# Kernel optimization log

Measured on AMD Instinct MI355X. Metric: run time of the kernel, lower is better.

Reference implementation:

```python
import math
import jax, jax.numpy as jnp
import numpy as np

H = 16  # num_attention_heads
EPS = 1e-6

def _rmsnorm(x, w):
    xf = x.astype(jnp.float32)
    y = xf * jax.lax.rsqrt(jnp.mean(xf * xf, axis=-1, keepdims=True) + EPS)
    return (y * w).astype(x.dtype)

def setup_inputs() -> dict:
    key = jax.random.key(0)
    ks = jax.random.split(key, 4)
    B, S, D = 4, 1536, 2048
    return {
        "x": jax.random.normal(ks[0], (B, S, D), jnp.float32),
        "w_qkv": jax.random.normal(ks[1], (D, 3 * D), jnp.float32) * (1.0 / math.sqrt(D)),
        "b_qkv": jnp.zeros((3 * D,), jnp.float32),
        "q_ln_w": jnp.ones((D,), jnp.float32),
        "k_ln_w": jnp.ones((D,), jnp.float32),
        "w_out": jax.random.normal(ks[2], (D, D), jnp.float32) * (1.0 / math.sqrt(D)),
        "b_out": jnp.zeros((D,), jnp.float32),
    }

def reference(x, w_qkv, b_qkv, q_ln_w, k_ln_w, w_out, b_out):
    B, S, D = x.shape
    hd = D // H
    scale = 1.0 / math.sqrt(hd)
    qkv = x @ w_qkv + b_qkv                     # [B,S,3D]
    q, k, v = jnp.split(qkv, 3, axis=-1)
    q = _rmsnorm(q, q_ln_w)                     # QK-RMSNorm over hidden dim
    k = _rmsnorm(k, k_ln_w)
    # [B,S,D] -> [B,H,S,hd]
    q = q.reshape(B, S, H, hd).transpose(0, 2, 1, 3)
    k = k.reshape(B, S, H, hd).transpose(0, 2, 1, 3)
    v = v.reshape(B, S, H, hd).transpose(0, 2, 1, 3)
    scores = jnp.einsum('bhqd,bhkd->bhqk', q, k) * scale
    min_val = jnp.finfo(scores.dtype).min
    causal = jnp.tril(jnp.ones((S, S), dtype=bool))
    scores = jnp.where(causal[None, None], scores, min_val)
    probs = jax.nn.softmax(scores, axis=-1)
    out = jnp.einsum('bhqk,bhkd->bhqd', probs, v)
    out = out.transpose(0, 2, 1, 3).reshape(B, S, D)
    return out @ w_out + b_out
```

## Files before the change

### kernel.cpp

```cpp
#include <hip/hip_runtime.h>
#include <stdint.h>

#define BB 4
#define SS 1536
#define DD 2048
#define HH 16
#define HD 128
#define BS (BB * SS)
#define N3 (3 * DD)

typedef __bf16 bf16x8 __attribute__((ext_vector_type(8)));
typedef float f32x4 __attribute__((ext_vector_type(4)));

__device__ __forceinline__ void async16(const void* g, void* lds) {
  __builtin_amdgcn_global_load_lds(
      (const __attribute__((address_space(1))) unsigned int*)g,
      (__attribute__((address_space(3))) unsigned int*)lds, 16, 0, 0);
}

__global__ __launch_bounds__(256) void cast_bf16_kernel(
    const float* __restrict__ in, __bf16* __restrict__ out) {
  long i = ((long)blockIdx.x * 256 + threadIdx.x) * 8;
  float4 a = *(const float4*)(in + i);
  float4 b = *(const float4*)(in + i + 4);
  bf16x8 o;
  o[0] = (__bf16)a.x; o[1] = (__bf16)a.y; o[2] = (__bf16)a.z; o[3] = (__bf16)a.w;
  o[4] = (__bf16)b.x; o[5] = (__bf16)b.y; o[6] = (__bf16)b.z; o[7] = (__bf16)b.w;
  *(bf16x8*)(out + i) = o;
}

__global__ __launch_bounds__(256) void transpose_cast_kernel(
    const float* __restrict__ in, __bf16* __restrict__ out, int R, int C) {
  __shared__ __bf16 t[32][33];
  int tx = threadIdx.x & 31, ty = threadIdx.x >> 5;
  long r0 = (long)blockIdx.y * 32, c0 = (long)blockIdx.x * 32;
#pragma unroll
  for (int i = 0; i < 4; ++i)
    t[ty + i * 8][tx] = (__bf16)in[(r0 + ty + i * 8) * C + c0 + tx];
  __syncthreads();
#pragma unroll
  for (int i = 0; i < 4; ++i)
    out[(c0 + ty + i * 8) * R + r0 + tx] = t[tx][ty + i * 8];
}

__device__ __forceinline__ void store_val(__bf16* p, float v) { *p = (__bf16)v; }
__device__ __forceinline__ void store_val(float* p, float v) { *p = v; }

#define MFMA_PRE()                                          \
  __builtin_amdgcn_s_barrier();                             \
  asm volatile("s_waitcnt lgkmcnt(0)" ::: "memory");        \
  __builtin_amdgcn_sched_barrier(0);                        \
  __builtin_amdgcn_s_setprio(1)
#define MFMA_POST()                                         \
  __builtin_amdgcn_s_setprio(0);                            \
  __builtin_amdgcn_s_barrier()
#define MFMA16(AF, BF, IOFF, JOFF)                                          \
  _Pragma("unroll") for (int i_ = 0; i_ < 4; ++i_)                          \
  _Pragma("unroll") for (int j_ = 0; j_ < 2; ++j_)                          \
  _Pragma("unroll") for (int kk_ = 0; kk_ < 2; ++kk_)                       \
    acc[(IOFF) + i_][(JOFF) + j_] = __builtin_amdgcn_mfma_f32_16x16x32_bf16( \
        AF[i_][kk_], BF[j_][kk_], acc[(IOFF) + i_][(JOFF) + j_], 0, 0, 0)

template <typename OutT>
__global__ __launch_bounds__(512, 2) void gemm256_kernel(
    const __bf16* __restrict__ A, const __bf16* __restrict__ Bt,
    const float* __restrict__ bias, OutT* __restrict__ C,
    int M, int N, int K) {
  __shared__ __attribute__((aligned(16))) __bf16 sA[2][2][128 * 64];
  __shared__ __attribute__((aligned(16))) __bf16 sB[2][2][128 * 64];

  const int tid = threadIdx.x;
  const int wave = tid >> 6, lane = tid & 63;
  const int quad = lane >> 4, l15 = lane & 15;
  const int s7 = l15 & 7;
  const int wm = wave >> 2, wn = wave & 3;

  const int nwg = gridDim.x;
  int wg = (int)blockIdx.x;
  wg = (wg & 7) * (nwg >> 3) + (wg >> 3);
  const int NB = N >> 8;
  const int bm = (wg / NB) << 8;
  const int bn = (wg % NB) << 8;

  const int srow = lane >> 3;
  const int schunk = (lane & 7) ^ srow;
  const __bf16* aSrc[2][2];
  const __bf16* bSrc[2][2];
#pragma unroll
  for (int h = 0; h < 2; ++h)
#pragma unroll
    for (int t8 = 0; t8 < 2; ++t8) {
      int rl = wave * 16 + t8 * 8 + srow;
      aSrc[h][t8] = A + (long)(bm + h * 128 + rl) * K + schunk * 8;
      bSrc[h][t8] = Bt + (long)(bn + h * 128 + rl) * K + schunk * 8;
    }

  auto stageA = [&](int kt, int b, int h) {
#pragma unroll
    for (int t8 = 0; t8 < 2; ++t8)
      async16(aSrc[h][t8] + kt * 64, &sA[b][h][(wave * 16 + t8 * 8) * 64]);
  };
  auto stageB = [&](int kt, int b, int h) {
#pragma unroll
    for (int t8 = 0; t8 < 2; ++t8)
      async16(bSrc[h][t8] + kt * 64, &sB[b][h][(wave * 16 + t8 * 8) * 64]);
  };
  auto readA = [&](int b, int i, int kk) -> bf16x8 {
    return *(const bf16x8*)&sA[b][wm]
        [(i * 16 + l15) * 64 + (((kk * 4 + quad) ^ s7) * 8)];
  };
  auto readB = [&](int b, int j, int kk) -> bf16x8 {
    return *(const bf16x8*)&sB[b][wn >> 1]
        [((wn & 1) * 64 + j * 16 + l15) * 64 + (((kk * 4 + quad) ^ s7) * 8)];
  };

  f32x4 acc[8][4] = {};

  stageA(0, 0, 0); stageA(0, 0, 1); stageB(0, 0, 0); stageB(0, 0, 1);
  stageA(1, 1, 0); stageA(1, 1, 1); stageB(1, 1, 0);
  asm volatile("s_waitcnt vmcnt(6)" ::: "memory");
  __builtin_amdgcn_s_barrier();

  const int NT = K >> 6;
  bf16x8 af[4][2], af2[4][2], bf[2][2], bf2[2][2];

#pragma unroll 1
  for (int t = 0; t < NT; t += 2) {
    const bool full = (t + 2) < NT;

#pragma unroll
    for (int i = 0; i < 4; ++i) { af[i][0] = readA(0, i, 0); af[i][1] = readA(0, i, 1); }
#pragma unroll
    for (int j = 0; j < 2; ++j) { bf[j][0] = readB(0, j, 0); bf[j][1] = readB(0, j, 1); }
    stageB(t + 1, 1, 1);
    MFMA_PRE();
    MFMA16(af, bf, 0, 0);
    MFMA_POST();

#pragma unroll
    for (int i = 0; i < 4; ++i) { af2[i][0] = readA(0, 4 + i, 0); af2[i][1] = readA(0, 4 + i, 1); }
    MFMA_PRE();
    MFMA16(af2, bf, 4, 0);
    MFMA_POST();

#pragma unroll
    for (int j = 0; j < 2; ++j) { bf2[j][0] = readB(0, 2 + j, 0); bf2[j][1] = readB(0, 2 + j, 1); }
    if (full) stageA(t + 2, 0, 0);
    MFMA_PRE();
    MFMA16(af2, bf2, 4, 2);
    MFMA_POST();

    if (full) {
      stageA(t + 2, 0, 1);
      stageB(t + 2, 0, 0);
      asm volatile("s_waitcnt vmcnt(6)" ::: "memory");
    } else {
      asm volatile("s_waitcnt vmcnt(0)" ::: "memory");
    }
    MFMA_PRE();
    MFMA16(af, bf2, 0, 2);
    MFMA_POST();

#pragma unroll
    for (int i = 0; i < 4; ++i) { af[i][0] = readA(1, i, 0); af[i][1] = readA(1, i, 1); }
#pragma unroll
    for (int j = 0; j < 2; ++j) { bf[j][0] = readB(1, j, 0); bf[j][1] = readB(1, j, 1); }
    if (full) stageB(t + 2, 0, 1);
    MFMA_PRE();
    MFMA16(af, bf, 0, 0);
    MFMA_POST();

#pragma unroll
    for (int i = 0; i < 4; ++i) { af2[i][0] = readA(1, 4 + i, 0); af2[i][1] = readA(1, 4 + i, 1); }
    MFMA_PRE();
    MFMA16(af2, bf, 4, 0);
    MFMA_POST();

#pragma unroll
    for (int j = 0; j < 2; ++j) { bf2[j][0] = readB(1, 2 + j, 0); bf2[j][1] = readB(1, 2 + j, 1); }
    if (full) stageA(t + 3, 1, 0);
    MFMA_PRE();
    MFMA16(af2, bf2, 4, 2);
    MFMA_POST();

    if (full) {
      stageA(t + 3, 1, 1);
      stageB(t + 3, 1, 0);
      asm volatile("s_waitcnt vmcnt(6)" ::: "memory");
    } else {
      asm volatile("s_waitcnt vmcnt(0)" ::: "memory");
    }
    MFMA_PRE();
    MFMA16(af, bf2, 0, 2);
    MFMA_POST();
  }

#pragma unroll
  for (int i = 0; i < 8; ++i) {
    int row0 = bm + wm * 128 + i * 16 + quad * 4;
#pragma unroll
    for (int j = 0; j < 4; ++j) {
      int col = bn + wn * 64 + j * 16 + l15;
      float bv = bias[col];
#pragma unroll
      for (int r = 0; r < 4; ++r)
        store_val(&C[(long)(row0 + r) * N + col], acc[i][j][r] + bv);
    }
  }
}

__global__ __launch_bounds__(256) void rmsnorm_kernel(
    __bf16* __restrict__ qkv, const float* __restrict__ qw,
    const float* __restrict__ kw) {
  const int r = blockIdx.x;
  const bool isQ = r < BS;
  const int row = isQ ? r : r - BS;
  __bf16* p = qkv + (long)row * N3 + (isQ ? 0 : DD);
  const float* w = isQ ? qw : kw;
  const float extra = isQ ? (0.0883883476483184f * 1.44269504088896f) : 1.0f;
  const int t = threadIdx.x;

  bf16x8 v = *(const bf16x8*)(p + t * 8);
  float f[8];
  float s = 0.f;
#pragma unroll
  for (int i = 0; i < 8; ++i) { f[i] = (float)v[i]; s += f[i] * f[i]; }
#pragma unroll
  for (int off = 32; off > 0; off >>= 1) s += __shfl_xor(s, off, 64);
  __shared__ float red[4];
  if ((t & 63) == 0) red[t >> 6] = s;
  __syncthreads();
  float tot = red[0] + red[1] + red[2] + red[3];
  float rs = rsqrtf(tot * (1.0f / (float)DD) + 1e-6f) * extra;
  bf16x8 o;
#pragma unroll
  for (int i = 0; i < 8; ++i) o[i] = (__bf16)(f[i] * rs * w[t * 8 + i]);
  *(bf16x8*)(p + t * 8) = o;
}

__global__ __launch_bounds__(256) void transpose_v_kernel(
    const __bf16* __restrict__ qkv, __bf16* __restrict__ vt) {
  __shared__ __bf16 t[32][33];
  const int bh = blockIdx.z, b = bh >> 4, h = bh & 15;
  const int s0 = blockIdx.x * 32, d0 = blockIdx.y * 32;
  const int tx = threadIdx.x & 31, ty = threadIdx.x >> 5;
#pragma unroll
  for (int i = 0; i < 4; ++i) {
    int s = s0 + ty + i * 8;
    t[ty + i * 8][tx] =
        qkv[(long)(b * SS + s) * N3 + 2 * DD + h * HD + d0 + tx];
  }
  __syncthreads();
#pragma unroll
  for (int i = 0; i < 4; ++i) {
    int d = d0 + ty + i * 8;
    vt[((long)bh * HD + d) * SS + s0 + tx] = t[tx][ty + i * 8];
  }
}

__global__ __launch_bounds__(256, 2) void attn_kernel(
    const __bf16* __restrict__ qkv, const __bf16* __restrict__ vt,
    __bf16* __restrict__ O) {
  __shared__ __attribute__((aligned(16))) __bf16 sK[2][64 * 128];
  __shared__ __attribute__((aligned(16))) __bf16 sV[2][128 * 64];
  __shared__ __attribute__((aligned(16))) __bf16 sP[4][32 * 64];

  const int qi = gridDim.x - 1 - blockIdx.x, bh = blockIdx.y;
  const int b = bh >> 4, h = bh & 15;
  const int tid = threadIdx.x, wave = tid >> 6, lane = tid & 63;
  const int quad = lane >> 4, l15 = lane & 15;
  const int sw3 = l15 & 7;

  const long rowQ0 = (long)(b * SS + qi * 128);
  const int qrow0 = qi * 128 + wave * 32;
  const __bf16* kbase = qkv + (long)(b * SS) * N3 + DD + h * HD;
  const __bf16* vbase = vt + (long)bh * HD * SS;

  bf16x8 qf[2][4];
#pragma unroll
  for (int mt = 0; mt < 2; ++mt) {
    const __bf16* qp =
        qkv + (rowQ0 + wave * 32 + mt * 16 + l15) * N3 + h * HD + quad * 8;
#pragma unroll
    for (int kk = 0; kk < 4; ++kk) qf[mt][kk] = *(const bf16x8*)(qp + kk * 32);
  }

  f32x4 o_acc[2][8] = {};
  float l_acc[2][4] = {};

  __bf16* sPw = &sP[wave][0];
  const int jn = 2 * qi + 2;

  auto stageKV = [&](int j, int buf) {
#pragma unroll
    for (int t = 0; t < 4; ++t) {
      int rbase = wave * 16 + t * 4;
      int row = rbase + quad;
      const __bf16* src =
          kbase + (long)(j * 64 + row) * N3 + ((l15 ^ (row & 7)) * 8);
      async16(src, &sK[buf][rbase * 128]);
    }
#pragma unroll
    for (int t = 0; t < 4; ++t) {
      int rbase = wave * 32 + t * 8;
      int row = rbase + (lane >> 3);
      const __bf16* src = vbase + (long)row * SS + j * 64 +
                          (((lane & 7) ^ (row & 7)) * 8);
      async16(src, &sV[buf][rbase * 64]);
    }
  };

  stageKV(0, 0);

  for (int j = 0; j < jn; ++j) {
    const int buf = j & 1;
    __syncthreads();
    if (j + 1 < jn) stageKV(j + 1, buf ^ 1);

    const bool active = !((j == 2 * qi + 1) && (wave < 2));
    if (active) {
      const bool needMask =
          ((j == 2 * qi) && (wave < 2)) || ((j == 2 * qi + 1) && (wave >= 2));

      f32x4 sacc[2][4];
#pragma unroll
      for (int nt = 0; nt < 4; ++nt) {
        sacc[0][nt] = (f32x4){0.f, 0.f, 0.f, 0.f};
        sacc[1][nt] = (f32x4){0.f, 0.f, 0.f, 0.f};
#pragma unroll
        for (int kk = 0; kk < 4; ++kk) {
          bf16x8 bk = *(const bf16x8*)
              &sK[buf][(nt * 16 + l15) * 128 + (((kk * 4 + quad) ^ sw3) * 8)];
          sacc[0][nt] = __builtin_amdgcn_mfma_f32_16x16x32_bf16(
              qf[0][kk], bk, sacc[0][nt], 0, 0, 0);
          sacc[1][nt] = __builtin_amdgcn_mfma_f32_16x16x32_bf16(
              qf[1][kk], bk, sacc[1][nt], 0, 0, 0);
        }
      }
      if (needMask) {
#pragma unroll
        for (int mt = 0; mt < 2; ++mt) {
          int rowg0 = qrow0 + mt * 16 + quad * 4;
#pragma unroll
          for (int nt = 0; nt < 4; ++nt) {
            int colg = j * 64 + nt * 16 + l15;
#pragma unroll
            for (int r = 0; r < 4; ++r)
              if (colg > rowg0 + r) sacc[mt][nt][r] = -1e30f;
          }
        }
      }
#pragma unroll
      for (int mt = 0; mt < 2; ++mt) {
#pragma unroll
        for (int nt = 0; nt < 4; ++nt) {
#pragma unroll
          for (int r = 0; r < 4; ++r) {
            float pv = exp2f(sacc[mt][nt][r]);
            l_acc[mt][r] += pv;
            int prow = mt * 16 + quad * 4 + r;
            int pcol = nt * 16 + l15;
            sPw[prow * 64 + (((pcol >> 3) ^ (prow & 7)) * 8) + (pcol & 7)] =
                (__bf16)pv;
          }
        }
      }
#pragma unroll
      for (int kk = 0; kk < 2; ++kk) {
        bf16x8 ap0 = *(const bf16x8*)
            &sPw[l15 * 64 + (((kk * 4 + quad) ^ sw3) * 8)];
        bf16x8 ap1 = *(const bf16x8*)
            &sPw[(16 + l15) * 64 + (((kk * 4 + quad) ^ sw3) * 8)];
#pragma unroll
        for (int dt = 0; dt < 8; ++dt) {
          bf16x8 bv = *(const bf16x8*)
              &sV[buf][(dt * 16 + l15) * 64 + (((kk * 4 + quad) ^ sw3) * 8)];
          o_acc[0][dt] = __builtin_amdgcn_mfma_f32_16x16x32_bf16(
              ap0, bv, o_acc[0][dt], 0, 0, 0);
          o_acc[1][dt] = __builtin_amdgcn_mfma_f32_16x16x32_bf16(
              ap1, bv, o_acc[1][dt], 0, 0, 0);
        }
      }
    }
  }

#pragma unroll
  for (int mt = 0; mt < 2; ++mt) {
    __bf16* obase = O + (rowQ0 + wave * 32 + mt * 16 + quad * 4) * DD + h * HD;
#pragma unroll
    for (int r = 0; r < 4; ++r) {
      float l = l_acc[mt][r];
#pragma unroll
      for (int off = 1; off < 16; off <<= 1) l += __shfl_xor(l, off, 64);
      float inv = 1.0f / l;
#pragma unroll
      for (int dt = 0; dt < 8; ++dt)
        obase[(long)r * DD + dt * 16 + l15] = (__bf16)(o_acc[mt][dt][r] * inv);
    }
  }
}

extern "C" void kernel_launch(void* const* d_in, const int* in_sizes, int n_in,
                              void* d_out, int out_size, void* d_ws,
                              size_t ws_size, hipStream_t stream) {
  const float* x      = (const float*)d_in[0];
  const float* w_qkv  = (const float*)d_in[1];
  const float* b_qkv  = (const float*)d_in[2];
  const float* q_ln_w = (const float*)d_in[3];
  const float* k_ln_w = (const float*)d_in[4];
  const float* w_out  = (const float*)d_in[5];
  const float* b_out  = (const float*)d_in[6];
  float* out = (float*)d_out;

  char* w = (char*)d_ws;
  __bf16* xb    = (__bf16*)(w);
  __bf16* wqkvT = (__bf16*)(w + 25165824L);
  __bf16* woutT = (__bf16*)(w + 50331648L);
  __bf16* qkvb  = (__bf16*)(w + 58720256L);
  __bf16* vtb   = (__bf16*)(w + 134217728L);
  __bf16* atto  = xb;

  cast_bf16_kernel<<<dim3(BS * DD / 2048), 256, 0, stream>>>(x, xb);
  transpose_cast_kernel<<<dim3(N3 / 32, DD / 32), 256, 0, stream>>>(
      w_qkv, wqkvT, DD, N3);
  transpose_cast_kernel<<<dim3(DD / 32, DD / 32), 256, 0, stream>>>(
      w_out, woutT, DD, DD);

  gemm256_kernel<__bf16><<<dim3((BS / 256) * (N3 / 256)), 512, 0, stream>>>(
      xb, wqkvT, b_qkv, qkvb, BS, N3, DD);

  rmsnorm_kernel<<<dim3(2 * BS), 256, 0, stream>>>(qkvb, q_ln_w, k_ln_w);

  transpose_v_kernel<<<dim3(SS / 32, HD / 32, BB * HH), 256, 0, stream>>>(
      qkvb, vtb);

  attn_kernel<<<dim3(SS / 128, BB * HH), 256, 0, stream>>>(qkvb, vtb, atto);

  gemm256_kernel<float><<<dim3((BS / 256) * (DD / 256)), 512, 0, stream>>>(
      atto, woutT, b_out, out, BS, DD, DD);
}
```

Baseline: 551.5 us.

## Software-pipeline LDS fragment reads across MFMA phases with partial lgkmcnt waits

Result: slower. 638.7 us (+15.8%).

```diff
diff --git a/kernel.cpp b/kernel.cpp
--- a/kernel.cpp
+++ b/kernel.cpp
@@ -46,18 +46,19 @@
 __device__ __forceinline__ void store_val(__bf16* p, float v) { *p = (__bf16)v; }
 __device__ __forceinline__ void store_val(float* p, float v) { *p = v; }
 
-#define MFMA_PRE()                                          \
-  __builtin_amdgcn_s_barrier();                             \
-  asm volatile("s_waitcnt lgkmcnt(0)" ::: "memory");        \
-  __builtin_amdgcn_sched_barrier(0);                        \
+#define PH_WAIT(N)                                              \
+  __builtin_amdgcn_s_barrier();                                 \
+  asm volatile("s_waitcnt lgkmcnt(" #N ")" ::: "memory");       \
+  __builtin_amdgcn_sched_barrier(0);                            \
   __builtin_amdgcn_s_setprio(1)
-#define MFMA_POST()                                         \
-  __builtin_amdgcn_s_setprio(0);                            \
-  __builtin_amdgcn_s_barrier()
-#define MFMA16(AF, BF, IOFF, JOFF)                                          \
-  _Pragma("unroll") for (int i_ = 0; i_ < 4; ++i_)                          \
-  _Pragma("unroll") for (int j_ = 0; j_ < 2; ++j_)                          \
-  _Pragma("unroll") for (int kk_ = 0; kk_ < 2; ++kk_)                       \
+#define PH_END()                                                \
+  __builtin_amdgcn_s_setprio(0);                                \
+  __builtin_amdgcn_s_barrier();                                 \
+  __builtin_amdgcn_sched_barrier(0)
+#define MFMA16(AF, BF, IOFF, JOFF)                                           \
+  _Pragma("unroll") for (int i_ = 0; i_ < 4; ++i_)                           \
+  _Pragma("unroll") for (int j_ = 0; j_ < 2; ++j_)                           \
+  _Pragma("unroll") for (int kk_ = 0; kk_ < 2; ++kk_)                        \
     acc[(IOFF) + i_][(JOFF) + j_] = __builtin_amdgcn_mfma_f32_16x16x32_bf16( \
         AF[i_][kk_], BF[j_][kk_], acc[(IOFF) + i_][(JOFF) + j_], 0, 0, 0)
 
@@ -84,26 +85,20 @@
 
   const int srow = lane >> 3;
   const int schunk = (lane & 7) ^ srow;
-  const __bf16* aSrc[2][2];
-  const __bf16* bSrc[2][2];
-#pragma unroll
-  for (int h = 0; h < 2; ++h)
-#pragma unroll
-    for (int t8 = 0; t8 < 2; ++t8) {
-      int rl = wave * 16 + t8 * 8 + srow;
-      aSrc[h][t8] = A + (long)(bm + h * 128 + rl) * K + schunk * 8;
-      bSrc[h][t8] = Bt + (long)(bn + h * 128 + rl) * K + schunk * 8;
-    }
+  const __bf16* Abase = A + (long)bm * K;
+  const __bf16* Bbase = Bt + (long)bn * K;
+  const int soff0 = (wave * 16 + 0 + srow) * K + schunk * 8;
+  const int soff1 = (wave * 16 + 8 + srow) * K + schunk * 8;
 
   auto stageA = [&](int kt, int b, int h) {
-#pragma unroll
-    for (int t8 = 0; t8 < 2; ++t8)
-      async16(aSrc[h][t8] + kt * 64, &sA[b][h][(wave * 16 + t8 * 8) * 64]);
+    const __bf16* p = Abase + (long)h * 128 * K + kt * 64;
+    async16(p + soff0, &sA[b][h][(wave * 16 + 0) * 64]);
+    async16(p + soff1, &sA[b][h][(wave * 16 + 8) * 64]);
   };
   auto stageB = [&](int kt, int b, int h) {
-#pragma unroll
-    for (int t8 = 0; t8 < 2; ++t8)
-      async16(bSrc[h][t8] + kt * 64, &sB[b][h][(wave * 16 + t8 * 8) * 64]);
+    const __bf16* p = Bbase + (long)h * 128 * K + kt * 64;
+    async16(p + soff0, &sB[b][h][(wave * 16 + 0) * 64]);
+    async16(p + soff1, &sB[b][h][(wave * 16 + 8) * 64]);
   };
   auto readA = [&](int b, int i, int kk) -> bf16x8 {
     return *(const bf16x8*)&sA[b][wm]
@@ -115,84 +110,87 @@
   };
 
   f32x4 acc[8][4] = {};
+  bf16x8 af[4][2], ah[4][2], bl[2][2], bh[2][2];
 
   stageA(0, 0, 0); stageA(0, 0, 1); stageB(0, 0, 0); stageB(0, 0, 1);
   stageA(1, 1, 0); stageA(1, 1, 1); stageB(1, 1, 0);
   asm volatile("s_waitcnt vmcnt(6)" ::: "memory");
   __builtin_amdgcn_s_barrier();
+  __builtin_amdgcn_sched_barrier(0);
+#pragma unroll
+  for (int i = 0; i < 4; ++i) { af[i][0] = readA(0, i, 0); af[i][1] = readA(0, i, 1); }
+#pragma unroll
+  for (int j = 0; j < 2; ++j) { bl[j][0] = readB(0, j, 0); bl[j][1] = readB(0, j, 1); }
 
   const int NT = K >> 6;
-  bf16x8 af[4][2], af2[4][2], bf[2][2], bf2[2][2];
 
 #pragma unroll 1
   for (int t = 0; t < NT; t += 2) {
     const bool full = (t + 2) < NT;
 
 #pragma unroll
-    for (int i = 0; i < 4; ++i) { af[i][0] = readA(0, i, 0); af[i][1] = readA(0, i, 1); }
-#pragma unroll
-    for (int j = 0; j < 2; ++j) { bf[j][0] = readB(0, j, 0); bf[j][1] = readB(0, j, 1); }
+    for (int j = 0; j < 2; ++j) { bh[j][0] = readB(0, 2 + j, 0); bh[j][1] = readB(0, 2 + j, 1); }
     stageB(t + 1, 1, 1);
-    MFMA_PRE();
-    MFMA16(af, bf, 0, 0);
-    MFMA_POST();
-
-#pragma unroll
-    for (int i = 0; i < 4; ++i) { af2[i][0] = readA(0, 4 + i, 0); af2[i][1] = readA(0, 4 + i, 1); }
-    MFMA_PRE();
-    MFMA16(af2, bf, 4, 0);
-    MFMA_POST();
-
-#pragma unroll
-    for (int j = 0; j < 2; ++j) { bf2[j][0] = readB(0, 2 + j, 0); bf2[j][1] = readB(0, 2 + j, 1); }
-    if (full) stageA(t + 2, 0, 0);
-    MFMA_PRE();
-    MFMA16(af2, bf2, 4, 2);
-    MFMA_POST();
+    PH_WAIT(4);
+    MFMA16(af, bl, 0, 0);
+    PH_END();
+
+#pragma unroll
+    for (int i = 0; i < 4; ++i) { ah[i][0] = readA(0, 4 + i, 0); ah[i][1] = readA(0, 4 + i, 1); }
+    PH_WAIT(8);
+    MFMA16(af, bh, 0, 2);
+    PH_END();
+
+    PH_WAIT(0);
+    MFMA16(ah, bh, 4, 2);
+    PH_END();
 
     if (full) {
-      stageA(t + 2, 0, 1);
-      stageB(t + 2, 0, 0);
+      stageA(t + 2, 0, 0); stageA(t + 2, 0, 1); stageB(t + 2, 0, 0);
       asm volatile("s_waitcnt vmcnt(6)" ::: "memory");
     } else {
       asm volatile("s_waitcnt vmcnt(0)" ::: "memory");
     }
-    MFMA_PRE();
-    MFMA16(af, bf2, 0, 2);
-    MFMA_POST();
-
+    PH_WAIT(0);
+    MFMA16(ah, bl, 4, 0);
 #pragma unroll
     for (int i = 0; i < 4; ++i) { af[i][0] = readA(1, i, 0); af[i][1] = readA(1, i, 1); }
 #pragma unroll
-    for (int j = 0; j < 2; ++j) { bf[j][0] = readB(1, j, 0); bf[j][1] = readB(1, j, 1); }
+    for (int j = 0; j < 2; ++j) { bl[j][0] = readB(1, j, 0); bl[j][1] = readB(1, j, 1); }
+    PH_END();
+
+#pragma unroll
+    for (int j = 0; j < 2; ++j) { bh[j][0] = readB(1, 2 + j, 0); bh[j][1] = readB(1, 2 + j, 1); }
     if (full) stageB(t + 2, 0, 1);
-    MFMA_PRE();
-    MFMA16(af, bf, 0, 0);
-    MFMA_POST();
-
-#pragma unroll
-    for (int i = 0; i < 4; ++i) { af2[i][0] = readA(1, 4 + i, 0); af2[i][1] = readA(1, 4 + i, 1); }
-    MFMA_PRE();
-    MFMA16(af2, bf, 4, 0);
-    MFMA_POST();
-
-#pragma unroll
-    for (int j = 0; j < 2; ++j) { bf2[j][0] = readB(1, 2 + j, 0); bf2[j][1] = readB(1, 2 + j, 1); }
-    if (full) stageA(t + 3, 1, 0);
-    MFMA_PRE();
-    MFMA16(af2, bf2, 4, 2);
-    MFMA_POST();
+    PH_WAIT(4);
+    MFMA16(af, bl, 0, 0);
+    PH_END();
+
+#pragma unroll
+    for (int i = 0; i < 4; ++i) { ah[i][0] = readA(1, 4 + i, 0); ah[i][1] = readA(1, 4 + i, 1); }
+    PH_WAIT(8);
+    MFMA16(af, bh, 0, 2);
+    PH_END();
+
+    PH_WAIT(0);
+    MFMA16(ah, bh, 4, 2);
+    PH_END();
 
     if (full) {
-      stageA(t + 3, 1, 1);
-      stageB(t + 3, 1, 0);
+      stageA(t + 3, 1, 0); stageA(t + 3, 1, 1); stageB(t + 3, 1, 0);
       asm volatile("s_waitcnt vmcnt(6)" ::: "memory");
     } else {
       asm volatile("s_waitcnt vmcnt(0)" ::: "memory");
     }
-    MFMA_PRE();
-    MFMA16(af, bf2, 0, 2);
-    MFMA_POST();
+    PH_WAIT(0);
+    MFMA16(ah, bl, 4, 0);
+    if (full) {
+#pragma unroll
+      for (int i = 0; i < 4; ++i) { af[i][0] = readA(0, i, 0); af[i][1] = readA(0, i, 1); }
+#pragma unroll
+      for (int j = 0; j < 2; ++j) { bl[j][0] = readB(0, j, 0); bl[j][1] = readB(0, j, 1); }
+    }
+    PH_END();
   }
 
 #pragma unroll
```
